# Kernel optimization log

Measured on AMD Instinct MI355X. Metric: run time of the kernel, lower is better.

Reference implementation:

```python
import jax, jax.numpy as jnp
import numpy as np

N = 50000      # total nodes
E = 800000     # edges
F = 256        # in_channels == per-layer out dim (output_dim // num_layers)
L = 3          # num_layers
MAXN = 512     # max_graph_size
B = 100        # graphs
EPS = 1e-5


def setup_inputs() -> dict:
    key = jax.random.key(0)
    ks = jax.random.split(key, 20)
    x = jax.random.normal(ks[0], (N, F), dtype=jnp.float32)
    edge_index = jax.random.randint(ks[1], (2, E), 0, N, dtype=jnp.int32)
    G = N // B
    batch = (jnp.arange(N, dtype=jnp.int32) // G).astype(jnp.int32)
    inp = {"x": x, "edge_index": edge_index, "batch": batch, "num_graphs": B}
    for i in range(L):
        s = 0.02
        inp[f"W{i}"] = jax.random.normal(ks[2 + 4 * i], (F, F), dtype=jnp.float32) * s
        inp[f"b{i}"] = jnp.zeros((F,), dtype=jnp.float32)
        inp[f"gamma{i}"] = jnp.ones((F,), dtype=jnp.float32)
        inp[f"beta{i}"] = jnp.zeros((F,), dtype=jnp.float32)
    return inp


def _gcn_norm(edge_index, n):
    # PyG GCNConv default: add self loops, symmetric normalization
    loop = jnp.arange(n, dtype=edge_index.dtype)
    src = jnp.concatenate([edge_index[0], loop])
    dst = jnp.concatenate([edge_index[1], loop])
    deg = jax.ops.segment_sum(jnp.ones_like(dst, dtype=jnp.float32), dst, num_segments=n)
    dinv = jnp.where(deg > 0, jax.lax.rsqrt(deg), 0.0)
    norm = dinv[src] * dinv[dst]  # [E+N]
    return src, dst, norm


def _gcn_conv(h, W, b, src, dst, norm, n):
    h = h @ W                                  # [N,F] dense linear
    msg = h[src] * norm[:, None]               # gather + edge normalize
    out = jax.ops.segment_sum(msg, dst, num_segments=n)  # scatter-add
    return out + b


def _bn_relu(h, gamma, beta):
    mu = jnp.mean(h, axis=0)
    var = jnp.var(h, axis=0)  # biased, as torch BN uses for normalization
    hn = (h - mu) * jax.lax.rsqrt(var + EPS) * gamma + beta
    return jax.nn.relu(hn)


def reference(x, edge_index, batch, num_graphs,
              W0, b0, gamma0, beta0,
              W1, b1, gamma1, beta1,
              W2, b2, gamma2, beta2):
    n = x.shape[0]
    src, dst, norm = _gcn_norm(edge_index, n)
    params = [(W0, b0, gamma0, beta0), (W1, b1, gamma1, beta1), (W2, b2, gamma2, beta2)]
    outs = []
    h = x
    for (W, b, g, be) in params:
        h = _gcn_conv(h, W, b, src, dst, norm, n)
        h = _bn_relu(h, g, be)
        outs.append(h)
    xcat = jnp.concatenate(outs, axis=-1)  # [N, 3F]
    # to_dense_batch: batch is sorted; position within graph
    counts = jax.ops.segment_sum(jnp.ones((n,), jnp.int32), batch, num_segments=num_graphs)
    starts = jnp.concatenate([jnp.zeros((1,), jnp.int32), jnp.cumsum(counts)[:-1]])
    pos = jnp.arange(n, dtype=jnp.int32) - starts[batch]
    dense = jnp.zeros((num_graphs, MAXN, xcat.shape[-1]), xcat.dtype)
    dense = dense.at[batch, pos].set(xcat)  # [B, max_nodes, output_dim]
    return dense
```

## Files before the change

### kernel.cpp

```cpp
#include <hip/hip_runtime.h>

typedef short bf16x8 __attribute__((ext_vector_type(8)));
typedef float f32x4 __attribute__((ext_vector_type(4)));

__device__ inline float bf2f(unsigned short s){ union{unsigned u; float f;} x; x.u=((unsigned)s)<<16; return x.f; }
__device__ inline unsigned short f2bf(float f){ union{float f; unsigned u;} x; x.f=f; unsigned r = x.u + 0x7fff + ((x.u>>16)&1u); return (unsigned short)(r>>16); }

__device__ inline void nt_store4(float4 v, float4* p){
    f32x4 t; t[0]=v.x; t[1]=v.y; t[2]=v.z; t[3]=v.w;
    __builtin_nontemporal_store(t, (f32x4*)p);
}

__device__ inline void gload16(const void* g, void* ldsbase){
    __builtin_amdgcn_global_load_lds((const __attribute__((address_space(1))) unsigned int*)g,
                                     (__attribute__((address_space(3))) unsigned int*)ldsbase, 16, 0, 0);
}

__global__ void k_hist_cvt(const int* __restrict__ dstA, int* __restrict__ cnt, int E, int histBlocks,
                           const float4* __restrict__ x4, ushort4* __restrict__ hb, int n4){
    int b = blockIdx.x;
    if(b < histBlocks){
        int e = b*256 + threadIdx.x;
        if(e < E) atomicAdd(&cnt[dstA[e]], 1);
    } else {
        int i = (b - histBlocks)*256 + threadIdx.x;
        if(i < n4){
            float4 v = x4[i];
            hb[i] = make_ushort4(f2bf(v.x), f2bf(v.y), f2bf(v.z), f2bf(v.w));
        }
    }
}

__global__ void k_scan1(const int* __restrict__ cnt, int* __restrict__ tmp, int* __restrict__ bsum,
                        float* __restrict__ dinv, int n){
    __shared__ int s[1024];
    int i = blockIdx.x*1024 + threadIdx.x;
    int v = (i < n) ? cnt[i] : 0;
    if(i < n) dinv[i] = rsqrtf((float)(v + 1));
    s[threadIdx.x] = v; __syncthreads();
    for(int off=1; off<1024; off<<=1){
        int t = (threadIdx.x >= off) ? s[threadIdx.x-off] : 0;
        __syncthreads();
        s[threadIdx.x] += t;
        __syncthreads();
    }
    if(i < n) tmp[i] = s[threadIdx.x];
    if(threadIdx.x == 1023) bsum[blockIdx.x] = s[1023];
}

__global__ void k_scan3_misc(const int* __restrict__ tmp, const int* __restrict__ bsum, int* __restrict__ rowptr,
                             int n, int gN, int nbScan,
                             const float* __restrict__ W0, const float* __restrict__ W1, const float* __restrict__ W2,
                             unsigned short* __restrict__ Wt, float4* __restrict__ out4, int G){
    int b = blockIdx.x;
    if(b < gN){
        __shared__ int pfx[64];
        if(threadIdx.x < 64){
            int v = ((int)threadIdx.x < nbScan) ? bsum[threadIdx.x] : 0;
            #pragma unroll
            for(int off=1; off<64; off<<=1){
                int t = __shfl_up(v, off, 64);
                if((int)threadIdx.x >= off) v += t;
            }
            pfx[threadIdx.x] = v;
        }
        __syncthreads();
        int i = b*256 + threadIdx.x;
        if(i < n){
            int blk = i >> 10;
            int p = (blk == 0) ? 0 : pfx[blk-1];
            rowptr[i+1] = tmp[i] + p;
            if(i == 0) rowptr[0] = 0;
        }
    } else if(b < gN + 768){
        int idx = (b - gN)*256 + threadIdx.x;
        int l = idx >> 16, rem = idx & 65535;
        int k = rem >> 8, nn = rem & 255;
        const float* W = (l==0) ? W0 : ((l==1) ? W1 : W2);
        Wt[l*65536 + nn*256 + k] = f2bf(W[k*256 + nn]);
    } else {
        int i = (b - gN - 768)*256 + threadIdx.x;
        int rowsPad = 512 - G;
        int per = rowsPad * 192;
        int total = 100 * per;
        if(i < total){
            int g = i / per; int rem = i - g*per;
            int r = rem / 192, c = rem - r*192;
            nt_store4(make_float4(0.f,0.f,0.f,0.f), &out4[((size_t)(g*512 + G + r))*192 + c]);
        }
    }
}

__global__ void k_fill(const int* __restrict__ srcA, const int* __restrict__ dstA,
                       const int* __restrict__ rowptr, int* __restrict__ cnt,
                       const float* __restrict__ dinv, int2* __restrict__ cew, int E){
    int e = blockIdx.x*256 + threadIdx.x;
    if(e < E){
        int d = dstA[e], s = srcA[e];
        int slot = atomicSub(&cnt[d], 1) - 1;
        int j = rowptr[d] + slot;
        cew[j] = make_int2(s, __float_as_int(dinv[s]));
    }
}

__global__ __launch_bounds__(256) void k_gemm(const uint4* __restrict__ A4,
                                              const uint4* __restrict__ B4,
                                              unsigned short* __restrict__ Y, int M){
    __shared__ uint4 smA[1024];
    __shared__ uint4 smB[1024];
    const int tid  = threadIdx.x;
    const int lane = tid & 63;
    const int w    = tid >> 6;
    const int wr   = w >> 1, wc = w & 1;
    const int r15  = lane & 15, hi = lane >> 4;
    const int rsub = lane >> 3, ch = lane & 7;
    const int rowBase = blockIdx.x * 128;
    const int colBase = blockIdx.y * 128;

    f32x4 acc[4][4] = {};
    char* pA = (char*)smA;
    char* pB = (char*)smB;

    for(int kt=0; kt<4; ++kt){
        const int kc0 = kt*8;
        #pragma unroll
        for(int i=0;i<4;++i){
            int row  = i*32 + w*8 + rsub;
            int gch  = kc0 + (ch ^ (row & 7));
            char* la = pA + i*4096 + w*1024;
            char* lb = pB + i*4096 + w*1024;
            int grow = rowBase + row;
            if(grow < M) gload16(&A4[(size_t)grow*32 + gch], la);
            gload16(&B4[(size_t)(colBase + row)*32 + gch], lb);
        }
        __syncthreads();
        #pragma unroll
        for(int kk=0; kk<2; ++kk){
            const int kbyte = kk*64 + hi*16;
            bf16x8 fa[4], fb[4];
            #pragma unroll
            for(int m=0;m<4;++m){
                int lrow = wr*64 + m*16 + r15;
                fa[m] = *(const bf16x8*)(pA + (lrow<<7) + (kbyte ^ ((lrow&7)<<4)));
            }
            #pragma unroll
            for(int nn=0;nn<4;++nn){
                int lcol = wc*64 + nn*16 + r15;
                fb[nn] = *(const bf16x8*)(pB + (lcol<<7) + (kbyte ^ ((lcol&7)<<4)));
            }
            #pragma unroll
            for(int m=0;m<4;++m)
                #pragma unroll
                for(int nn=0;nn<4;++nn)
                    acc[m][nn] = __builtin_amdgcn_mfma_f32_16x16x32_bf16(fa[m], fb[nn], acc[m][nn], 0,0,0);
        }
        __syncthreads();
    }
    #pragma unroll
    for(int m=0;m<4;++m){
        int growb = rowBase + wr*64 + m*16 + hi*4;
        #pragma unroll
        for(int nn=0;nn<4;++nn){
            int gcol = colBase + wc*64 + nn*16 + r15;
            #pragma unroll
            for(int r=0;r<4;++r){
                int grow = growb + r;
                if(grow < M) Y[(size_t)grow*256 + gcol] = f2bf(acc[m][nn][r]);
            }
        }
    }
}

__global__ __launch_bounds__(256) void k_aggregate(const uint4* __restrict__ yb4,
                                                   const int* __restrict__ rowptr,
                                                   const int2* __restrict__ cew,
                                                   const float* __restrict__ dinv,
                                                   uint4* __restrict__ zb4,
                                                   float* __restrict__ part, int n){
    int lane = threadIdx.x & 63;
    int w    = threadIdx.x >> 6;
    int half = lane >> 5;
    int c    = lane & 31;
    float s[8] = {0,0,0,0,0,0,0,0};
    float q[8] = {0,0,0,0,0,0,0,0};

    for(int wid = blockIdx.x*4 + w; wid < n; wid += 2048*4){
        float di = dinv[wid];
        float acc[4][8];
        {
            uint4 d = yb4[(size_t)wid*32 + c];
            float ws = half ? 0.f : di;
            const unsigned short* p = (const unsigned short*)&d;
            #pragma unroll
            for(int k=0;k<8;++k) acc[0][k] = ws*bf2f(p[k]);
            #pragma unroll
            for(int k=0;k<8;++k){ acc[1][k]=0.f; acc[2][k]=0.f; acc[3][k]=0.f; }
        }
        int j = rowptr[wid], end = rowptr[wid+1];
        for(; j+7 < end; j += 8){
            #pragma unroll
            for(int u=0;u<4;++u){
                int2 e = cew[j + 2*u + half];
                float wt = __int_as_float(e.y);
                uint4 d = yb4[(size_t)e.x*32 + c];
                const unsigned short* p = (const unsigned short*)&d;
                #pragma unroll
                for(int k=0;k<8;++k) acc[u][k] += wt*bf2f(p[k]);
            }
        }
        for(; j+1 < end; j += 2){
            int2 e = cew[j + half];
            float wt = __int_as_float(e.y);
            uint4 d = yb4[(size_t)e.x*32 + c];
            const unsigned short* p = (const unsigned short*)&d;
            #pragma unroll
            for(int k=0;k<8;++k) acc[0][k] += wt*bf2f(p[k]);
        }
        if(j < end){
            int2 e = cew[j];
            float wt = half ? 0.f : __int_as_float(e.y);
            uint4 d = yb4[(size_t)e.x*32 + c];
            const unsigned short* p = (const unsigned short*)&d;
            #pragma unroll
            for(int k=0;k<8;++k) acc[0][k] += wt*bf2f(p[k]);
        }
        float o[8];
        #pragma unroll
        for(int k=0;k<8;++k){
            float v = (acc[0][k]+acc[1][k]) + (acc[2][k]+acc[3][k]);
            v += __shfl(v, lane ^ 32);
            o[k] = di * v;
        }
        if(half == 0){
            uint4 z;
            z.x = (unsigned)f2bf(o[0]) | ((unsigned)f2bf(o[1])<<16);
            z.y = (unsigned)f2bf(o[2]) | ((unsigned)f2bf(o[3])<<16);
            z.z = (unsigned)f2bf(o[4]) | ((unsigned)f2bf(o[5])<<16);
            z.w = (unsigned)f2bf(o[6]) | ((unsigned)f2bf(o[7])<<16);
            zb4[(size_t)wid*32 + c] = z;
            #pragma unroll
            for(int k=0;k<8;++k){ s[k] += o[k]; q[k] += o[k]*o[k]; }
        }
    }
    __shared__ float red[4][32][16];
    if(half == 0){
        #pragma unroll
        for(int k=0;k<8;++k){ red[w][c][k] = s[k]; red[w][c][8+k] = q[k]; }
    }
    __syncthreads();
    int t = threadIdx.x;
    float vs = red[0][t>>3][t&7] + red[1][t>>3][t&7] + red[2][t>>3][t&7] + red[3][t>>3][t&7];
    float vq = red[0][t>>3][8+(t&7)] + red[1][t>>3][8+(t&7)] + red[2][t>>3][8+(t&7)] + red[3][t>>3][8+(t&7)];
    part[(size_t)blockIdx.x*512 + t]       = vs;
    part[(size_t)blockIdx.x*512 + 256 + t] = vq;
}

__global__ __launch_bounds__(256) void k_red1(const float* __restrict__ part, float* __restrict__ part2){
    int c = threadIdx.x;
    int b = blockIdx.x;
    float s = 0.f, q = 0.f;
    for(int j = b*32; j < b*32 + 32; ++j){
        s += part[(size_t)j*512 + c];
        q += part[(size_t)j*512 + 256 + c];
    }
    part2[(size_t)b*512 + c]       = s;
    part2[(size_t)b*512 + 256 + c] = q;
}

__global__ __launch_bounds__(256) void k_red2(const float* __restrict__ part2,
                                              const float* __restrict__ gamma, const float* __restrict__ beta,
                                              float* __restrict__ ab, float invN){
    int c = threadIdx.x;
    float s = 0.f, q = 0.f;
    for(int j=0;j<64;++j){
        s += part2[(size_t)j*512 + c];
        q += part2[(size_t)j*512 + 256 + c];
    }
    float mu  = s*invN;
    float var = q*invN - mu*mu;
    float A   = gamma[c]*rsqrtf(var + 1e-5f);
    ab[c]       = A;
    ab[256 + c] = beta[c] - mu*A;
}

__global__ __launch_bounds__(256) void k_bnrelu(const ushort4* __restrict__ zb, const float* __restrict__ ab,
                                                ushort4* __restrict__ hb_out, float4* __restrict__ out4,
                                                int layer, int n4, int G){
    int idx = blockIdx.x*256 + threadIdx.x;
    if(idx >= n4) return;
    int node = idx >> 6, q = idx & 63;
    ushort4 v = zb[idx];
    float4 A  = ((const float4*)ab)[q];
    float4 Bv = ((const float4*)(ab + 256))[q];
    float4 r;
    r.x = fmaxf(fmaf(bf2f(v.x), A.x, Bv.x), 0.f);
    r.y = fmaxf(fmaf(bf2f(v.y), A.y, Bv.y), 0.f);
    r.z = fmaxf(fmaf(bf2f(v.z), A.z, Bv.z), 0.f);
    r.w = fmaxf(fmaf(bf2f(v.w), A.w, Bv.w), 0.f);
    if(hb_out) hb_out[idx] = make_ushort4(f2bf(r.x), f2bf(r.y), f2bf(r.z), f2bf(r.w));
    int g2 = node / G;
    int p  = node - g2*G;
    nt_store4(r, &out4[((size_t)(g2*512 + p))*192 + layer*64 + q]);
}

extern "C" void kernel_launch(void* const* d_in, const int* in_sizes, int n_in,
                              void* d_out, int out_size, void* d_ws, size_t ws_size,
                              hipStream_t stream){
    const int F = 256;
    const int N = in_sizes[0] / F;
    const int E = in_sizes[1] / 2;
    const int Bg = 100;
    const int G = N / Bg;

    const float* x  = (const float*)d_in[0];
    const int*   ei = (const int*)d_in[1];
    const float* Wp[3]  = {(const float*)d_in[4],  (const float*)d_in[8],  (const float*)d_in[12]};
    const float* gam[3] = {(const float*)d_in[6],  (const float*)d_in[10], (const float*)d_in[14]};
    const float* bet[3] = {(const float*)d_in[7],  (const float*)d_in[11], (const float*)d_in[15]};
    float* out = (float*)d_out;

    char* wp = (char*)d_ws;
    auto alloc = [&](size_t b)->char*{ char* p = wp; wp += ((b + 255)/256)*256; return p; };
    int*   cnt    = (int*)  alloc((size_t)N*4);
    int*   rowptr = (int*)  alloc((size_t)(N+1)*4);
    int*   tmp    = (int*)  alloc((size_t)N*4);
    int*   bsum   = (int*)  alloc(256*4);
    int2*  cew    = (int2*) alloc((size_t)E*8);
    float* dinv   = (float*)alloc((size_t)N*4);
    float* part   = (float*)alloc((size_t)2048*512*4);
    float* part2  = (float*)alloc((size_t)64*512*4);
    float* ab     = (float*)alloc(3*512*4);
    unsigned short* Wt  = (unsigned short*)alloc(3*65536*2);
    unsigned short* hbA = (unsigned short*)alloc((size_t)N*256*2);
    unsigned short* hbB = (unsigned short*)alloc((size_t)N*256*2);
    unsigned short* ybf = (unsigned short*)alloc((size_t)N*256*2);
    unsigned short* zb  = (unsigned short*)alloc((size_t)N*256*2);

    (void)hipMemsetAsync(cnt, 0, (size_t)N*4, stream);

    const int* srcA = ei;
    const int* dstA = ei + E;
    int gE = (E+255)/256, gN = (N+255)/256;
    int n4 = N*64;
    int nbCvt = (n4+255)/256;
    k_hist_cvt<<<gE + nbCvt, 256, 0, stream>>>(dstA, cnt, E, gE, (const float4*)x, (ushort4*)hbA, n4);
    int nb = (N+1023)/1024;
    k_scan1<<<nb,1024,0,stream>>>(cnt, tmp, bsum, dinv, N);
    int padBlocks = (Bg*(512-G)*192 + 255)/256;
    k_scan3_misc<<<gN + 768 + padBlocks, 256, 0, stream>>>(tmp, bsum, rowptr, N, gN, nb,
                                                           Wp[0], Wp[1], Wp[2], Wt, (float4*)out, G);
    k_fill<<<gE,256,0,stream>>>(srcA, dstA, rowptr, cnt, dinv, cew, E);

    unsigned short* hin  = hbA;
    unsigned short* hout = hbB;
    dim3 ggrid((N+127)/128, 2);
    float invN = 1.0f / (float)N;
    for(int l=0; l<3; ++l){
        float* lab = ab + l*512;
        k_gemm<<<ggrid,256,0,stream>>>((const uint4*)hin, (const uint4*)(Wt + (size_t)l*65536), ybf, N);
        k_aggregate<<<2048,256,0,stream>>>((const uint4*)ybf, rowptr, cew, dinv, (uint4*)zb, part, N);
        k_red1<<<64,256,0,stream>>>(part, part2);
        k_red2<<<1,256,0,stream>>>(part2, gam[l], bet[l], lab, invN);
        k_bnrelu<<<(n4+255)/256,256,0,stream>>>((const ushort4*)zb, lab,
                                                (l<2) ? (ushort4*)hout : (ushort4*)nullptr,
                                                (float4*)out, l, n4, G);
        unsigned short* t = hin; hin = hout; hout = t;
    }
}
```

Before: 420.1 us.

## Widen GEMM tile to full 256 columns and fuse BN reduction kernels

The GEMM now computes all 256 output columns per block (128x256 tile) instead of splitting columns across two grid blocks. Each A tile is therefore loaded once, at the cost of doubled B LDS, twice the accumulator registers and half as many blocks. The two BN-statistics reduction kernels are merged into one, where the last-arriving block finalizes the scale/shift via an atomic counter with threadfences. This removes one launch per layer; the per-layer counters are cleared by the extended memset.

```diff
diff --git a/kernel.cpp b/kernel.cpp
--- a/kernel.cpp
+++ b/kernel.cpp
@@ -107,7 +107,7 @@
                                               const uint4* __restrict__ B4,
                                               unsigned short* __restrict__ Y, int M){
     __shared__ uint4 smA[1024];
-    __shared__ uint4 smB[1024];
+    __shared__ uint4 smB[2048];
     const int tid  = threadIdx.x;
     const int lane = tid & 63;
     const int w    = tid >> 6;
@@ -115,9 +115,8 @@
     const int r15  = lane & 15, hi = lane >> 4;
     const int rsub = lane >> 3, ch = lane & 7;
     const int rowBase = blockIdx.x * 128;
-    const int colBase = blockIdx.y * 128;
-
-    f32x4 acc[4][4] = {};
+
+    f32x4 acc[4][8] = {};
     char* pA = (char*)smA;
     char* pB = (char*)smB;
 
@@ -128,31 +127,34 @@
             int row  = i*32 + w*8 + rsub;
             int gch  = kc0 + (ch ^ (row & 7));
             char* la = pA + i*4096 + w*1024;
-            char* lb = pB + i*4096 + w*1024;
             int grow = rowBase + row;
             if(grow < M) gload16(&A4[(size_t)grow*32 + gch], la);
-            gload16(&B4[(size_t)(colBase + row)*32 + gch], lb);
+        }
+        #pragma unroll
+        for(int i=0;i<8;++i){
+            int row  = i*32 + w*8 + rsub;
+            int gch  = kc0 + (ch ^ (row & 7));
+            char* lb = pB + i*4096 + w*1024;
+            gload16(&B4[(size_t)row*32 + gch], lb);
         }
         __syncthreads();
         #pragma unroll
         for(int kk=0; kk<2; ++kk){
             const int kbyte = kk*64 + hi*16;
-            bf16x8 fa[4], fb[4];
+            bf16x8 fa[4];
             #pragma unroll
             for(int m=0;m<4;++m){
                 int lrow = wr*64 + m*16 + r15;
                 fa[m] = *(const bf16x8*)(pA + (lrow<<7) + (kbyte ^ ((lrow&7)<<4)));
             }
             #pragma unroll
-            for(int nn=0;nn<4;++nn){
-                int lcol = wc*64 + nn*16 + r15;
-                fb[nn] = *(const bf16x8*)(pB + (lcol<<7) + (kbyte ^ ((lcol&7)<<4)));
-            }
-            #pragma unroll
-            for(int m=0;m<4;++m)
+            for(int nn=0;nn<8;++nn){
+                int lcol = wc*128 + nn*16 + r15;
+                bf16x8 fb = *(const bf16x8*)(pB + (lcol<<7) + (kbyte ^ ((lcol&7)<<4)));
                 #pragma unroll
-                for(int nn=0;nn<4;++nn)
-                    acc[m][nn] = __builtin_amdgcn_mfma_f32_16x16x32_bf16(fa[m], fb[nn], acc[m][nn], 0,0,0);
+                for(int m=0;m<4;++m)
+                    acc[m][nn] = __builtin_amdgcn_mfma_f32_16x16x32_bf16(fa[m], fb, acc[m][nn], 0,0,0);
+            }
         }
         __syncthreads();
     }
@@ -160,8 +162,8 @@
     for(int m=0;m<4;++m){
         int growb = rowBase + wr*64 + m*16 + hi*4;
         #pragma unroll
-        for(int nn=0;nn<4;++nn){
-            int gcol = colBase + wc*64 + nn*16 + r15;
+        for(int nn=0;nn<8;++nn){
+            int gcol = wc*128 + nn*16 + r15;
             #pragma unroll
             for(int r=0;r<4;++r){
                 int grow = growb + r;
@@ -255,7 +257,9 @@
     part[(size_t)blockIdx.x*512 + 256 + t] = vq;
 }
 
-__global__ __launch_bounds__(256) void k_red1(const float* __restrict__ part, float* __restrict__ part2){
+__global__ __launch_bounds__(256) void k_red(const float* __restrict__ part, float* __restrict__ part2,
+                                             const float* __restrict__ gamma, const float* __restrict__ beta,
+                                             float* __restrict__ ab, float invN, int* __restrict__ ctr){
     int c = threadIdx.x;
     int b = blockIdx.x;
     float s = 0.f, q = 0.f;
@@ -265,22 +269,28 @@
     }
     part2[(size_t)b*512 + c]       = s;
     part2[(size_t)b*512 + 256 + c] = q;
-}
-
-__global__ __launch_bounds__(256) void k_red2(const float* __restrict__ part2,
-                                              const float* __restrict__ gamma, const float* __restrict__ beta,
-                                              float* __restrict__ ab, float invN){
-    int c = threadIdx.x;
-    float s = 0.f, q = 0.f;
-    for(int j=0;j<64;++j){
-        s += part2[(size_t)j*512 + c];
-        q += part2[(size_t)j*512 + 256 + c];
-    }
-    float mu  = s*invN;
-    float var = q*invN - mu*mu;
-    float A   = gamma[c]*rsqrtf(var + 1e-5f);
-    ab[c]       = A;
-    ab[256 + c] = beta[c] - mu*A;
+
+    __threadfence();
+    __syncthreads();
+    __shared__ int lastFlag;
+    if(threadIdx.x == 0){
+        int old = atomicAdd(ctr, 1);
+        lastFlag = (old == 63);
+    }
+    __syncthreads();
+    if(lastFlag){
+        __threadfence();
+        float ss = 0.f, qq = 0.f;
+        for(int j=0;j<64;++j){
+            ss += part2[(size_t)j*512 + c];
+            qq += part2[(size_t)j*512 + 256 + c];
+        }
+        float mu  = ss*invN;
+        float var = qq*invN - mu*mu;
+        float A   = gamma[c]*rsqrtf(var + 1e-5f);
+        ab[c]       = A;
+        ab[256 + c] = beta[c] - mu*A;
+    }
 }
 
 __global__ __launch_bounds__(256) void k_bnrelu(const ushort4* __restrict__ zb, const float* __restrict__ ab,
@@ -322,6 +332,7 @@
     char* wp = (char*)d_ws;
     auto alloc = [&](size_t b)->char*{ char* p = wp; wp += ((b + 255)/256)*256; return p; };
     int*   cnt    = (int*)  alloc((size_t)N*4);
+    int*   ctr    = (int*)  alloc(256);
     int*   rowptr = (int*)  alloc((size_t)(N+1)*4);
     int*   tmp    = (int*)  alloc((size_t)N*4);
     int*   bsum   = (int*)  alloc(256*4);
@@ -336,7 +347,8 @@
     unsigned short* ybf = (unsigned short*)alloc((size_t)N*256*2);
     unsigned short* zb  = (unsigned short*)alloc((size_t)N*256*2);
 
-    (void)hipMemsetAsync(cnt, 0, (size_t)N*4, stream);
+    size_t cntRound = (((size_t)N*4 + 255)/256)*256;
+    (void)hipMemsetAsync(cnt, 0, cntRound + 256, stream);
 
     const int* srcA = ei;
     const int* dstA = ei + E;
@@ -353,14 +365,13 @@
 
     unsigned short* hin  = hbA;
     unsigned short* hout = hbB;
-    dim3 ggrid((N+127)/128, 2);
+    int ggrid = (N+127)/128;
     float invN = 1.0f / (float)N;
     for(int l=0; l<3; ++l){
         float* lab = ab + l*512;
         k_gemm<<<ggrid,256,0,stream>>>((const uint4*)hin, (const uint4*)(Wt + (size_t)l*65536), ybf, N);
         k_aggregate<<<2048,256,0,stream>>>((const uint4*)ybf, rowptr, cew, dinv, (uint4*)zb, part, N);
-        k_red1<<<64,256,0,stream>>>(part, part2);
-        k_red2<<<1,256,0,stream>>>(part2, gam[l], bet[l], lab, invN);
+        k_red<<<64,256,0,stream>>>(part, part2, gam[l], bet[l], lab, invN, ctr + l);
         k_bnrelu<<<(n4+255)/256,256,0,stream>>>((const ushort4*)zb, lab,
                                                 (l<2) ? (ushort4*)hout : (ushort4*)nullptr,
                                                 (float4*)out, l, n4, G);
```

New measurement: 443.8 us. 1.06x slower.
